# Kernel optimization log

Hardware: AMD Instinct MI355X
Metric: run time of the kernel (lower is better)

## Reference

```python
import jax, jax.numpy as jnp
import numpy as np

DIM = 1024
H = 16
HKV = 4
HD = DIM // H  # 64
GROUP = H // HKV
ROPE_BASE = 10000.0
B, T = 2, 2048


def rms_norm(x, eps):
    return x * jax.lax.rsqrt(jnp.mean(x * x, axis=-1, keepdims=True) + eps)


def apply_rotary(x, cos, sin):
    # x: [B, h, T, HD]; cos/sin: [1, 1, T, HD//2]
    half = x.shape[-1] // 2
    x1, x2 = x[..., :half], x[..., half:]
    return jnp.concatenate([x1 * cos + x2 * sin, -x1 * sin + x2 * cos], axis=-1)


def setup_inputs() -> dict:
    key = jax.random.key(0)
    ks = jax.random.split(key, 5)
    s = 0.02
    return {
        "x": jax.random.normal(ks[0], (B, T, DIM), dtype=jnp.float32),
        "Wq": jax.random.normal(ks[1], (DIM, DIM), dtype=jnp.float32) * s,
        "Wk": jax.random.normal(ks[2], (HKV * HD, DIM), dtype=jnp.float32) * s,
        "Wv": jax.random.normal(ks[3], (HKV * HD, DIM), dtype=jnp.float32) * s,
        "Wproj": jax.random.normal(ks[4], (DIM, DIM), dtype=jnp.float32) * s,
        "q_gain": jnp.full((H,), 12.0, dtype=jnp.float32),
    }


def reference(x, Wq, Wk, Wv, Wproj, q_gain):
    bsz, seqlen, dim = x.shape
    eps = jnp.asarray(jnp.finfo(x.dtype).eps, x.dtype)

    # double RMSNorm path: normalized input for q/k, raw input for v
    x_qk = rms_norm(x, eps)
    q = (x_qk @ Wq.T).reshape(bsz, seqlen, H, HD).transpose(0, 2, 1, 3)    # [B,H,T,D]
    k = (x_qk @ Wk.T).reshape(bsz, seqlen, HKV, HD).transpose(0, 2, 1, 3)  # [B,Hkv,T,D]
    v = (x @ Wv.T).reshape(bsz, seqlen, HKV, HD).transpose(0, 2, 1, 3)     # [B,Hkv,T,D]

    q = rms_norm(q, eps)
    k = rms_norm(k, eps)

    # rotary embeddings
    t = jnp.arange(seqlen, dtype=jnp.float32)
    inv_freq = 1.0 / (ROPE_BASE ** (jnp.arange(0, HD, 2, dtype=jnp.float32) / HD))
    freqs = jnp.outer(t, inv_freq)                       # [T, HD//2]
    cos = jnp.cos(freqs)[None, None].astype(x.dtype)
    sin = jnp.sin(freqs)[None, None].astype(x.dtype)
    q = apply_rotary(q, cos, sin)
    k = apply_rotary(k, cos, sin)

    # per-head gain on q
    q = q * q_gain.astype(q.dtype)[None, :, None, None]

    # GQA: expand kv heads to query heads
    k_r = jnp.repeat(k, GROUP, axis=1)  # [B,H,T,D]
    v_r = jnp.repeat(v, GROUP, axis=1)

    scale = 1.0 / np.sqrt(HD)
    scores = jnp.einsum("bhqd,bhkd->bhqk", q, k_r) * scale
    causal = jnp.tril(jnp.ones((seqlen, seqlen), dtype=bool))
    scores = jnp.where(causal[None, None], scores, jnp.asarray(-jnp.inf, scores.dtype))
    attn = jax.nn.softmax(scores, axis=-1)
    y = jnp.einsum("bhqk,bhkd->bhqd", attn, v_r)          # [B,H,T,D]

    # XSA: remove value-direction component from output
    y_bt = y.transpose(0, 2, 1, 3)                        # [B,T,H,D]
    v_bt = v.transpose(0, 2, 1, 3)                        # [B,T,Hkv,D]
    y_g = y_bt.reshape(bsz, seqlen, HKV, GROUP, HD)
    vnorm = jnp.sqrt(jnp.sum(v_bt * v_bt, axis=-1, keepdims=True))
    vn = (v_bt / jnp.maximum(vnorm, 1e-12))[..., None, :]  # [B,T,Hkv,1,D]
    proj = jnp.sum(y_g * vn, axis=-1, keepdims=True) * vn
    y_bt = (y_g - proj).reshape(bsz, seqlen, H, HD)

    return y_bt.reshape(bsz, seqlen, dim) @ Wproj.T
```

## Files before the change

kernel.cpp:

```cpp
#include <hip/hip_runtime.h>
#include <hip/hip_bf16.h>

typedef __attribute__((ext_vector_type(8))) short bf8v;
typedef __attribute__((ext_vector_type(4))) float f4v;
typedef __attribute__((ext_vector_type(4))) unsigned u4v;

#define MFMA16(a,b,c) __builtin_amdgcn_mfma_f32_16x16x32_bf16((a),(b),(c),0,0,0)

#define GLD16(gp, lp) __builtin_amdgcn_global_load_lds( \
    (const __attribute__((address_space(1))) void*)(gp), \
    (__attribute__((address_space(3))) void*)(lp), 16, 0, 0)

#define DIMC   1024
#define TSEQ   2048
#define NH     16
#define NKV    4
#define HDIM   64
#define RMS_EPS 1.1920929e-07f
#define QSCALE 0.1803368801111601f

__device__ __forceinline__ ushort f2bf(float f) {
  unsigned u = __builtin_bit_cast(unsigned, f);
  u = (u + 0x7FFFu + ((u >> 16) & 1u)) >> 16;
  return (ushort)u;
}
__device__ __forceinline__ float bf2f(ushort u) {
  return __builtin_bit_cast(float, (unsigned)u << 16);
}
__device__ __forceinline__ unsigned cvtpk(float lo, float hi) {
  unsigned r;
  asm("v_cvt_pk_bf16_f32 %0, %1, %2" : "=v"(r) : "v"(lo), "v"(hi));
  return r;
}

__global__ __launch_bounds__(256) void prep_all(
    const float* __restrict__ x,
    const float* __restrict__ Wq, const float* __restrict__ Wk,
    const float* __restrict__ Wv, const float* __restrict__ Wp,
    ushort* __restrict__ xhi, ushort* __restrict__ xlo,
    ushort* __restrict__ xb,
    ushort* __restrict__ wqkh, ushort* __restrict__ wqkl,
    ushort* __restrict__ wvb, ushort* __restrict__ wpb,
    float* __restrict__ cosT, float* __restrict__ sinT) {
  __shared__ float red[4];
  int bid = blockIdx.x, tid = threadIdx.x;
  if (bid < 4096) {
    int row = bid;
    int lane = tid & 63, w = tid >> 6;
    float4 v = ((const float4*)(x + (size_t)row * DIMC))[tid];
    float ss = v.x * v.x + v.y * v.y + v.z * v.z + v.w * v.w;
    for (int off = 32; off; off >>= 1) ss += __shfl_xor(ss, off);
    if (lane == 0) red[w] = ss;
    __syncthreads();
    float tot = red[0] + red[1] + red[2] + red[3];
    float rs = rsqrtf(tot * (1.0f / DIMC) + RMS_EPS);
    float n0 = v.x * rs, n1 = v.y * rs, n2 = v.z * rs, n3 = v.w * rs;
    ushort4 h, l, ob;
    h.x = f2bf(n0); l.x = f2bf(n0 - bf2f(h.x));
    h.y = f2bf(n1); l.y = f2bf(n1 - bf2f(h.y));
    h.z = f2bf(n2); l.z = f2bf(n2 - bf2f(h.z));
    h.w = f2bf(n3); l.w = f2bf(n3 - bf2f(h.w));
    ob.x = f2bf(v.x); ob.y = f2bf(v.y); ob.z = f2bf(v.z); ob.w = f2bf(v.w);
    ((ushort4*)(xhi + (size_t)row * DIMC))[tid] = h;
    ((ushort4*)(xlo + (size_t)row * DIMC))[tid] = l;
    ((ushort4*)(xb  + (size_t)row * DIMC))[tid] = ob;
    return;
  }
  int wb = bid - 4096;
  if (wb < 1280) {
    const float* src;
    size_t si, di;
    if (wb < 1024) { src = Wq; si = (size_t)wb * 256 + tid; di = si; }
    else { src = Wk; si = (size_t)(wb - 1024) * 256 + tid; di = 262144 + si; }
    float4 v = ((const float4*)src)[si];
    ushort4 h, l;
    h.x = f2bf(v.x); l.x = f2bf(v.x - bf2f(h.x));
    h.y = f2bf(v.y); l.y = f2bf(v.y - bf2f(h.y));
    h.z = f2bf(v.z); l.z = f2bf(v.z - bf2f(h.z));
    h.w = f2bf(v.w); l.w = f2bf(v.w - bf2f(h.w));
    ((ushort4*)wqkh)[di] = h;
    ((ushort4*)wqkl)[di] = l;
  } else if (wb < 2560) {
    const float* src;
    ushort* dst;
    int i;
    if (wb < 1536) { src = Wv; dst = wvb; i = (wb - 1280) * 256 + tid; }
    else           { src = Wp; dst = wpb; i = (wb - 1536) * 256 + tid; }
    float4 v = ((const float4*)src)[i];
    ushort4 o;
    o.x = f2bf(v.x); o.y = f2bf(v.y); o.z = f2bf(v.z); o.w = f2bf(v.w);
    ((ushort4*)dst)[i] = o;
  } else {
    int i = (wb - 2560) * 256 + tid;
    int t = i >> 5, j = i & 31;
    float inv = 1.0f / powf(10000.0f, (float)j * (1.0f / 32.0f));
    float f = (float)t * inv;
    cosT[i] = cosf(f);
    sinT[i] = sinf(f);
  }
}

__global__ __launch_bounds__(256, 3)
void gemm_qkv(const ushort* __restrict__ xhi, const ushort* __restrict__ xlo,
              const ushort* __restrict__ wqkh, const ushort* __restrict__ wqkl,
              float* __restrict__ QKf, ushort* __restrict__ QKc,
              const ushort* __restrict__ xb, const ushort* __restrict__ wvb,
              float* __restrict__ Vf) {
  __shared__ __align__(16) ushort lA[128 * 64];
  __shared__ __align__(16) ushort lB[128 * 64];
  const int bid = blockIdx.x;
  int u;
  bool big;
  if (bid < 256)      { big = true;  u = bid; }
  else if (bid < 448) { big = false; u = bid - 256; }
  else if (bid < 512) { big = true;  u = 256 + (bid - 448); }
  else                { big = false; u = 192 + (bid - 512); }

  const ushort *Ap0, *Bp0, *Ap1, *Bp1;
  float* Cf = QKf;
  int N = 1280, nsteps, mt, n0;
  if (big) {
    mt = u / 10; n0 = (u % 10) * 128;
    Ap0 = xlo; Bp0 = wqkh; Ap1 = xhi; Bp1 = wqkl; nsteps = 32;
  } else if (u < 320) {
    mt = u / 10; n0 = (u % 10) * 128;
    Ap0 = xhi; Bp0 = wqkh; Ap1 = Ap0; Bp1 = Bp0; nsteps = 16;
  } else {
    int v = u - 320; mt = v >> 1; n0 = (v & 1) * 128;
    Ap0 = xb; Bp0 = wvb; Ap1 = Ap0; Bp1 = Bp0; nsteps = 16;
    Cf = Vf; N = 256;
  }
  const int m0 = mt * 128;

  const int t = threadIdx.x;
  const int lane = t & 63, w = t >> 6;
  const int wr = w >> 1, wc = w & 1;
  const int l15 = lane & 15, lg = lane >> 4;
  const int srow = t >> 3, scp = t & 7;

  f4v acc[4][4] = {};

  for (int s = 0; s < nsteps; ++s) {
    const ushort* Ab = (s < 16) ? Ap0 : Ap1;
    const ushort* Bb = (s < 16) ? Bp0 : Bp1;
    const int kk = (s & 15) * 64;
    for (int i = 0; i < 4; ++i) {
      int row = srow + i * 32;
      int sc = scp ^ (row & 7);
      const ushort* ga = Ab + (size_t)(m0 + row) * DIMC + kk + sc * 8;
      const ushort* gb = Bb + (size_t)(n0 + row) * DIMC + kk + sc * 8;
      GLD16(ga, &lA[w * 512 + i * 2048]);
      GLD16(gb, &lB[w * 512 + i * 2048]);
    }
    __syncthreads();
    for (int kx = 0; kx < 2; ++kx) {
      bf8v af[4], bfr[4];
      for (int m = 0; m < 4; ++m) {
        int row = wr * 64 + m * 16 + l15;
        int ch = (kx * 4 + lg) ^ (row & 7);
        af[m] = *(const bf8v*)&lA[row * 64 + ch * 8];
      }
      for (int n = 0; n < 4; ++n) {
        int row = wc * 64 + n * 16 + l15;
        int ch = (kx * 4 + lg) ^ (row & 7);
        bfr[n] = *(const bf8v*)&lB[row * 64 + ch * 8];
      }
      for (int m = 0; m < 4; ++m)
        for (int n = 0; n < 4; ++n)
          acc[m][n] = MFMA16(af[m], bfr[n], acc[m][n]);
    }
    __syncthreads();
  }

  if (big) {
    for (int m = 0; m < 4; ++m)
      for (int n = 0; n < 4; ++n)
        for (int j = 0; j < 4; ++j) {
          int r = m0 + wr * 64 + m * 16 + lg * 4 + j;
          int c = n0 + wc * 64 + n * 16 + l15;
          QKc[(size_t)r * 1280 + c] = f2bf(acc[m][n][j]);
        }
  } else {
    for (int m = 0; m < 4; ++m)
      for (int n = 0; n < 4; ++n)
        for (int j = 0; j < 4; ++j) {
          int r = m0 + wr * 64 + m * 16 + lg * 4 + j;
          int c = n0 + wc * 64 + n * 16 + l15;
          Cf[(size_t)r * N + c] = acc[m][n][j];
        }
  }
}

__global__ __launch_bounds__(256, 2)
void gemm_bt(const ushort* __restrict__ A0, const ushort* __restrict__ B0,
             float* __restrict__ C, int N) {
  __shared__ __align__(16) ushort lA[128 * 64];
  __shared__ __align__(16) ushort lB[64 * 64];
  const int t = threadIdx.x;
  const int lane = t & 63, w = t >> 6;
  const int l15 = lane & 15, lg = lane >> 4;
  const int m0 = blockIdx.y * 128, n0 = blockIdx.x * 64;
  const int srow = t >> 3, scp = t & 7;

  f4v acc[2][4] = {};

  for (int k0 = 0; k0 < 1024; k0 += 64) {
    for (int i = 0; i < 4; ++i) {
      int row = srow + i * 32;
      int sc = scp ^ (row & 7);
      const ushort* ga = A0 + (size_t)(m0 + row) * DIMC + k0 + sc * 8;
      GLD16(ga, &lA[w * 512 + i * 2048]);
    }
    for (int i = 0; i < 2; ++i) {
      int row = srow + i * 32;
      int sc = scp ^ (row & 7);
      const ushort* gb = B0 + (size_t)(n0 + row) * DIMC + k0 + sc * 8;
      GLD16(gb, &lB[w * 512 + i * 2048]);
    }
    __syncthreads();
    for (int kx = 0; kx < 2; ++kx) {
      bf8v af[2], bfr[4];
      for (int m = 0; m < 2; ++m) {
        int row = w * 32 + m * 16 + l15;
        int ch = (kx * 4 + lg) ^ (row & 7);
        af[m] = *(const bf8v*)&lA[row * 64 + ch * 8];
      }
      for (int n = 0; n < 4; ++n) {
        int row = n * 16 + l15;
        int ch = (kx * 4 + lg) ^ (row & 7);
        bfr[n] = *(const bf8v*)&lB[row * 64 + ch * 8];
      }
      for (int m = 0; m < 2; ++m)
        for (int n = 0; n < 4; ++n)
          acc[m][n] = MFMA16(af[m], bfr[n], acc[m][n]);
    }
    __syncthreads();
  }

  for (int m = 0; m < 2; ++m)
    for (int n = 0; n < 4; ++n)
      for (int j = 0; j < 4; ++j) {
        int r = m0 + w * 32 + m * 16 + lg * 4 + j;
        int c = n0 + n * 16 + l15;
        C[(size_t)r * N + c] = acc[m][n][j];
      }
}

__global__ __launch_bounds__(256) void post_all(
    const float* __restrict__ QKf, const ushort* __restrict__ QKc,
    const float* __restrict__ cosT,
    const float* __restrict__ sinT, const float* __restrict__ qgain,
    ushort* __restrict__ qhi, ushort* __restrict__ qlo,
    ushort* __restrict__ kb16,
    const float* __restrict__ Vf, ushort* __restrict__ vt2,
    ushort* __restrict__ vhat_q) {
  __shared__ float lds[64][69];
  __shared__ float rnv[64];
  int bid = blockIdx.x;
  if (bid < 4096) {
    int m = bid;
    int b = m >> 11, tpos = m & 2047;
    int lane = threadIdx.x & 63, w = threadIdx.x >> 6;
    int d = lane, j = d & 31;
    float sgn = (d < 32) ? 1.0f : -1.0f;
    float c = cosT[tpos * 32 + j], s = sinT[tpos * 32 + j];

    for (int i = 0; i < 4; ++i) {
      int h = w * 4 + i;
      size_t base = (size_t)m * 1280 + h * HDIM + d;
      float q = QKf[base] + bf2f(QKc[base]);
      float ss = q * q;
      for (int off = 32; off; off >>= 1) ss += __shfl_xor(ss, off);
      float rs = rsqrtf(ss * (1.0f / HDIM) + RMS_EPS);
      float qn = q * rs;
      float partner = __shfl_xor(qn, 32);
      float ro = (qn * c + sgn * partner * s) * (qgain[h] * QSCALE);
      ushort hi = f2bf(ro);
      ushort lo = f2bf(ro - bf2f(hi));
      size_t idx = (((size_t)b * NH + h) * TSEQ + tpos) * HDIM + d;
      qhi[idx] = hi;
      qlo[idx] = lo;
    }
    {
      int kv = w;
      size_t base = (size_t)m * 1280 + 1024 + kv * HDIM + d;
      float k = QKf[base] + bf2f(QKc[base]);
      float ss = k * k;
      for (int off = 32; off; off >>= 1) ss += __shfl_xor(ss, off);
      float rs = rsqrtf(ss * (1.0f / HDIM) + RMS_EPS);
      float kn = k * rs;
      float partner = __shfl_xor(kn, 32);
      float ro = kn * c + sgn * partner * s;
      kb16[((size_t)(b * NKV + kv) * TSEQ + tpos) * HDIM + d] = f2bf(ro);
    }
    return;
  }
  {
    int vb = bid - 4096;
    int bkv = vb >> 5, tt = vb & 31;
    int b = bkv >> 2, kv = bkv & 3;
    int tid = threadIdx.x;
    for (int i = 0; i < 16; ++i) {
      int idx = i * 256 + tid;
      int tloc = idx >> 6, d = idx & 63;
      lds[d][tloc] = Vf[((size_t)(b * TSEQ + tt * 64 + tloc)) * 256 + kv * 64 + d];
    }
    __syncthreads();
    {
      int t = tid >> 2, prt = tid & 3;
      float ssum = 0.f;
      for (int dd = 0; dd < 16; ++dd) {
        float v = lds[prt * 16 + dd][t];
        ssum += v * v;
      }
      ssum += __shfl_xor(ssum, 1);
      ssum += __shfl_xor(ssum, 2);
      if (prt == 0) rnv[t] = 1.0f / fmaxf(sqrtf(ssum), 1e-12f);
    }
    __syncthreads();
    for (int i = 0; i < 16; ++i) {
      int idx = i * 256 + tid;
      int d = idx >> 6, tloc = idx & 63;
      vt2[(size_t)bkv * (TSEQ * 64) + tt * 4096 + d * 64 + tloc] = f2bf(lds[d][tloc]);
    }
    for (int i = 0; i < 16; ++i) {
      int idx = i * 256 + tid;
      int tloc = idx >> 6, d = idx & 63;
      vhat_q[((size_t)bkv * TSEQ + tt * 64 + tloc) * 64 + d] =
          f2bf(lds[d][tloc] * rnv[tloc]);
    }
  }
}

#define E(s,t,k,l) ((unsigned)(s) | ((unsigned)(t) << 8) | \
                    ((unsigned)(k) << 16) | ((unsigned)(l) << 24))
__global__ __launch_bounds__(256, 5) void attn_chunk(
    const ushort* __restrict__ qhi, const ushort* __restrict__ qlo,
    const ushort* __restrict__ kb16, const ushort* __restrict__ vt2,
    ushort* __restrict__ pyb, float* __restrict__ pml) {
  static const unsigned LUT[80] = {
    E(76,31,0,8), E(77,31,8,8), E(78,31,16,8), E(79,31,24,8),
    E(72,30,0,8), E(73,30,8,8), E(74,30,16,8),
    E(68,29,0,8), E(69,29,8,8), E(64,28,0,8),
    E(45,23,0,8), E(46,23,8,8), E(47,23,16,8),
    E(42,22,0,8), E(43,22,8,8), E(39,21,0,8),
    E(22,15,0,8), E(23,15,8,8), E(20,14,0,8), E(7,7,0,8),
    E(75,30,24,7), E(70,29,16,7), E(71,29,23,7),
    E(65,28,8,7), E(66,28,15,7), E(67,28,22,7),
    E(60,27,0,7), E(61,27,7,7), E(62,27,14,7), E(63,27,21,7),
    E(56,26,0,7), E(57,26,7,7), E(58,26,14,7),
    E(52,25,0,7), E(53,25,7,7), E(48,24,0,7),
    E(44,22,16,7), E(40,21,8,7), E(41,21,15,7),
    E(36,20,0,7), E(37,20,7,7), E(38,20,14,7),
    E(33,19,0,7), E(34,19,7,7), E(30,18,0,7),
    E(21,14,8,7), E(18,13,0,7), E(19,13,7,7), E(16,12,0,7), E(6,6,0,7),
    E(59,26,21,6), E(54,25,14,6), E(55,25,20,6),
    E(49,24,7,6), E(50,24,13,6), E(51,24,19,6),
    E(35,19,14,6), E(31,18,7,6), E(32,18,13,6),
    E(27,17,0,6), E(28,17,6,6), E(29,17,12,6),
    E(24,16,0,6), E(25,16,6,6),
    E(17,12,7,6), E(14,11,0,6), E(15,11,6,6), E(12,10,0,6), E(5,5,0,6),
    E(26,16,12,5), E(13,10,6,5), E(10,9,0,5), E(11,9,5,5),
    E(8,8,0,5), E(4,4,0,5),
    E(9,8,5,4), E(3,3,0,4),
    E(2,2,0,3), E(1,1,0,2), E(0,0,0,1)
  };
  __shared__ __align__(16) ushort lk[2][64 * 64];
  __shared__ __align__(16) ushort lv[2][64 * 64];
  const int t = threadIdx.x;
  const int lane = t & 63, w = t >> 6;
  const int bid = blockIdx.x;
  const int combo = bid & 31;
  const unsigned e = LUT[bid >> 5];
  const int slot = e & 255;
  const int tile = (e >> 8) & 31;
  const int kb0 = (e >> 16) & 31;
  const int len = (int)(e >> 24);

  const int xcd = combo & 7, g = (combo >> 3) & 3;
  const int b = xcd >> 2, kv = xcd & 3, h = kv * 4 + g;
  const int l15 = lane & 15, lg = lane >> 4;
  const int q0 = tile * 64 + w * 16;
  const int t3 = t >> 3, tc8 = t & 7;
  const int rx = l15 & 7;
  const bool odd = (lg & 1);

  const size_t qoff = (((size_t)(b * NH + h)) * TSEQ + q0 + l15) * HDIM;
  bf8v bq0h = *(const bf8v*)(qhi + qoff + lg * 8);
  bf8v bq1h = *(const bf8v*)(qhi + qoff + 32 + lg * 8);
  bf8v bq0l = *(const bf8v*)(qlo + qoff + lg * 8);
  bf8v bq1l = *(const bf8v*)(qlo + qoff + 32 + lg * 8);

  const ushort* kb = kb16 + (size_t)(b * NKV + kv) * TSEQ * 64;
  const ushort* vb = vt2 + (size_t)(b * NKV + kv) * TSEQ * 64;

#define STAGE(BUF, KT) do { \
    _Pragma("unroll") \
    for (int i = 0; i < 2; ++i) { \
      int row = i * 32 + t3; \
      int sc = tc8 ^ (row & 7); \
      GLD16(kb + (size_t)((KT) * 64 + row) * 64 + sc * 8, \
            &lk[BUF][(i * 32 + (w << 3)) * 64]); \
      GLD16(vb + (size_t)(KT) * 4096 + row * 64 + sc * 8, \
            &lv[BUF][(i * 32 + (w << 3)) * 64]); \
    } } while (0)

  STAGE(0, kb0);

  f4v y[4] = {};
  float mrow = -1e30f, lrow = 0.f;

#pragma unroll 1
  for (int itc = 0; itc < len; ++itc) {
    const int cur = itc & 1;
    const int kt = kb0 + itc;
    __syncthreads();
    if (itc + 1 < len) STAGE(cur ^ 1, kt + 1);

    const ushort* lkc = &lk[cur][0];
    const ushort* lvc = &lv[cur][0];
    const int kv0 = kt * 64;

    f4v s4[4];
    __builtin_amdgcn_s_setprio(1);
#pragma unroll
    for (int n = 0; n < 4; ++n) {
      const ushort* krow = lkc + (n * 16 + l15) * 64;
      bf8v kh0 = *(const bf8v*)&krow[((0 + lg) ^ rx) * 8];
      bf8v kh1 = *(const bf8v*)&krow[((4 + lg) ^ rx) * 8];
      f4v z = {};
      f4v acc = MFMA16(kh0, bq0h, z);
      acc = MFMA16(kh1, bq1h, acc);
      acc = MFMA16(kh0, bq0l, acc);
      acc = MFMA16(kh1, bq1l, acc);
      s4[n] = acc;
    }
    __builtin_amdgcn_s_setprio(0);

    const bool need_mask = (kt == tile);
    float mloc = -1e30f;
#pragma unroll
    for (int n = 0; n < 4; ++n)
#pragma unroll
      for (int j = 0; j < 4; ++j) {
        float v = s4[n][j];
        if (need_mask && (kv0 + n * 16 + lg * 4 + j > q0 + l15)) v = -1e30f;
        s4[n][j] = v;
        mloc = fmaxf(mloc, v);
      }
    if (__any(mloc > mrow + 11.5f)) {
      float mf = fmaxf(mloc, __shfl_xor(mloc, 16));
      mf = fmaxf(mf, __shfl_xor(mf, 32));
      float mnew = fmaxf(mrow, mf);
      float scf = exp2f(mrow - mnew);
      lrow *= scf;
#pragma unroll
      for (int n = 0; n < 4; ++n) y[n] *= scf;
      mrow = mnew;
    }
#pragma unroll
    for (int n = 0; n < 4; ++n)
#pragma unroll
      for (int j = 0; j < 4; ++j) {
        float e2 = exp2f(s4[n][j] - mrow);
        s4[n][j] = e2;
        lrow += e2;
      }

    unsigned d0a = cvtpk(s4[0][0], s4[0][1]), d0b = cvtpk(s4[0][2], s4[0][3]);
    unsigned d1a = cvtpk(s4[1][0], s4[1][1]), d1b = cvtpk(s4[1][2], s4[1][3]);
    unsigned d2a = cvtpk(s4[2][0], s4[2][1]), d2b = cvtpk(s4[2][2], s4[2][3]);
    unsigned d3a = cvtpk(s4[3][0], s4[3][1]), d3b = cvtpk(s4[3][2], s4[3][3]);
    asm("v_permlane32_swap_b32 %0, %1" : "+v"(d0a), "+v"(d1a));
    asm("v_permlane32_swap_b32 %0, %1" : "+v"(d0b), "+v"(d1b));
    asm("v_permlane32_swap_b32 %0, %1" : "+v"(d2a), "+v"(d3a));
    asm("v_permlane32_swap_b32 %0, %1" : "+v"(d2b), "+v"(d3b));
    unsigned sa0 = (unsigned)__shfl_xor((int)d0a, 16);
    unsigned sb0 = (unsigned)__shfl_xor((int)d1a, 16);
    unsigned sa1 = (unsigned)__shfl_xor((int)d0b, 16);
    unsigned sb1 = (unsigned)__shfl_xor((int)d1b, 16);
    unsigned sa2 = (unsigned)__shfl_xor((int)d2a, 16);
    unsigned sb2 = (unsigned)__shfl_xor((int)d3a, 16);
    unsigned sa3 = (unsigned)__shfl_xor((int)d2b, 16);
    unsigned sb3 = (unsigned)__shfl_xor((int)d3b, 16);
    u4v u0 = { odd ? sb0 : d0a, odd ? sb1 : d0b,
               odd ? d1a : sa0, odd ? d1b : sa1 };
    u4v u1 = { odd ? sb2 : d2a, odd ? sb3 : d2b,
               odd ? d3a : sa2, odd ? d3b : sa3 };
    bf8v pb0 = __builtin_bit_cast(bf8v, u0);
    bf8v pb1 = __builtin_bit_cast(bf8v, u1);

    __builtin_amdgcn_s_setprio(1);
#pragma unroll
    for (int n = 0; n < 4; ++n) {
      const ushort* vrow = lvc + (n * 16 + l15) * 64;
      bf8v va0 = *(const bf8v*)&vrow[((0 + lg) ^ rx) * 8];
      bf8v va1 = *(const bf8v*)&vrow[((4 + lg) ^ rx) * 8];
      y[n] = MFMA16(va0, pb0, y[n]);
      y[n] = MFMA16(va1, pb1, y[n]);
    }
    __builtin_amdgcn_s_setprio(0);
  }
#undef STAGE

  {
    lrow += __shfl_xor(lrow, 16);
    lrow += __shfl_xor(lrow, 32);
    const int pslot = combo * 80 + slot;
    ushort* pb = pyb + (size_t)pslot * 4096;
    const int q = w * 16 + l15;
#pragma unroll
    for (int n = 0; n < 4; ++n) {
      uint2 pk;
      pk.x = cvtpk(y[n][0], y[n][1]);
      pk.y = cvtpk(y[n][2], y[n][3]);
      *(uint2*)&pb[q * 64 + n * 16 + lg * 4] = pk;
    }
    if (lane < 16) {
      float* mlp = pml + (size_t)pslot * 128;
      mlp[q] = mrow;
      mlp[64 + q] = lrow;
    }
  }
}
#undef E

__global__ __launch_bounds__(256) void combine_kern(
    const ushort* __restrict__ pyb, const float* __restrict__ pml,
    const ushort* __restrict__ vhat_q, ushort* __restrict__ ytil) {
  const int bid = blockIdx.x;
  const int combo = bid & 31, tile = bid >> 5;
  const int xcd = combo & 7, g = (combo >> 3) & 3;
  const int b = xcd >> 2, kv = xcd & 3, h = kv * 4 + g;
  const int nch = (tile + 8) >> 3;
  const int sb = (tile < 8) ? tile
               : (tile < 16) ? 8 + ((tile - 8) << 1)
               : (tile < 24) ? 24 + 3 * (tile - 16)
                             : 48 + ((tile - 24) << 2);
  const int tid = threadIdx.x;
  const int q = tid >> 2, ds = (tid & 3) * 16;
  const int q0 = tile * 64;

  float m[4], l[4];
#pragma unroll
  for (int ci = 0; ci < 4; ++ci) {
    if (ci < nch) {
      const float* mlp = pml + (size_t)(combo * 80 + sb + ci) * 128;
      m[ci] = mlp[q];
      l[ci] = mlp[64 + q];
    } else { m[ci] = -1e30f; l[ci] = 0.f; }
  }
  float M = fmaxf(fmaxf(m[0], m[1]), fmaxf(m[2], m[3]));
  float y[16] = {};
  float ltot = 0.f;
#pragma unroll
  for (int ci = 0; ci < 4; ++ci) {
    if (ci < nch) {
      float sc = exp2f(m[ci] - M);
      ltot += l[ci] * sc;
      const ushort* pb = pyb + (size_t)(combo * 80 + sb + ci) * 4096 + q * 64 + ds;
      bf8v p0 = *(const bf8v*)pb;
      bf8v p1 = *(const bf8v*)(pb + 8);
#pragma unroll
      for (int dd = 0; dd < 8; ++dd) {
        y[dd] += sc * bf2f((ushort)p0[dd]);
        y[8 + dd] += sc * bf2f((ushort)p1[dd]);
      }
    }
  }
  float inv = 1.0f / ltot;
  const ushort* vh = vhat_q + ((size_t)(b * NKV + kv) * TSEQ + q0 + q) * 64 + ds;
  bf8v v0 = *(const bf8v*)vh;
  bf8v v1 = *(const bf8v*)(vh + 8);
  float vv[16];
  float dp = 0.f;
#pragma unroll
  for (int dd = 0; dd < 8; ++dd) {
    vv[dd] = bf2f((ushort)v0[dd]);
    vv[8 + dd] = bf2f((ushort)v1[dd]);
  }
#pragma unroll
  for (int dd = 0; dd < 16; ++dd) {
    y[dd] *= inv;
    dp += y[dd] * vv[dd];
  }
  dp += __shfl_xor(dp, 1);
  dp += __shfl_xor(dp, 2);
  bf8v o0, o1;
#pragma unroll
  for (int dd = 0; dd < 8; ++dd) {
    o0[dd] = (short)f2bf(y[dd] - dp * vv[dd]);
    o1[dd] = (short)f2bf(y[8 + dd] - dp * vv[8 + dd]);
  }
  ushort* yo = ytil + ((size_t)(b * TSEQ + q0 + q)) * DIMC + h * HDIM + ds;
  *(bf8v*)yo = o0;
  *(bf8v*)(yo + 8) = o1;
}

extern "C" void kernel_launch(void* const* d_in, const int* in_sizes, int n_in,
                              void* d_out, int out_size, void* d_ws, size_t ws_size,
                              hipStream_t stream) {
  (void)in_sizes; (void)n_in; (void)out_size; (void)ws_size;
  const float* x  = (const float*)d_in[0];
  const float* Wq = (const float*)d_in[1];
  const float* Wk = (const float*)d_in[2];
  const float* Wv = (const float*)d_in[3];
  const float* Wp = (const float*)d_in[4];
  const float* qg = (const float*)d_in[5];
  float* out = (float*)d_out;
  char* ws = (char*)d_ws;
  const size_t KB = 1024, MB = 1ull << 20;

  ushort* xhi = (ushort*)(ws);
  ushort* xlo = (ushort*)(ws + 8 * MB);
  ushort* xb  = (ushort*)(ws + 16 * MB);
  ushort* wqkh = (ushort*)(ws + 24 * MB);
  ushort* wqkl = (ushort*)(ws + 26 * MB + 512 * KB);
  ushort* wvb = (ushort*)(ws + 29 * MB);
  ushort* wpb = (ushort*)(ws + 29 * MB + 512 * KB);
  float*  cosT = (float*)(ws + 31 * MB + 512 * KB);
  float*  sinT = (float*)(ws + 31 * MB + 768 * KB);
  float*  QKf  = (float*)(ws + 32 * MB);
  ushort* kb16 = (ushort*)(ws + 52 * MB);
  ushort* vt2  = (ushort*)(ws + 54 * MB);

  float*  Vf   = out;
  ushort* QKc  = (ushort*)((char*)out + 4 * MB);
  ushort* vhat_q = (ushort*)((char*)out + 14 * MB);
  ushort* qhb  = xhi;
  ushort* qlb  = xlo;
  ushort* ytil = xb;
  ushort* pyb = (ushort*)(ws + 32 * MB);
  float*  pml = (float*)(ws + 56 * MB);

  prep_all<<<6912, 256, 0, stream>>>(x, Wq, Wk, Wv, Wp, xhi, xlo, xb,
                                     wqkh, wqkl, wvb, wpb, cosT, sinT);

  gemm_qkv<<<704, 256, 0, stream>>>(xhi, xlo, wqkh, wqkl, QKf, QKc,
                                    xb, wvb, Vf);

  post_all<<<4352, 256, 0, stream>>>(QKf, QKc, cosT, sinT, qg, qhb, qlb, kb16,
                                     Vf, vt2, vhat_q);
  attn_chunk<<<2560, 256, 0, stream>>>(qhb, qlb, kb16, vt2, pyb, pml);
  combine_kern<<<1024, 256, 0, stream>>>(pyb, pml, vhat_q, ytil);
  gemm_bt<<<dim3(16, 32), 256, 0, stream>>>(ytil, wpb, out, 1024);
}
```

Baseline: 141.9 us.

## Process two 64-row query tiles per attention block to reuse staged K/V

Result: slower. 220.3 us (+55.2%).

```diff
diff --git a/kernel.cpp b/kernel.cpp
--- a/kernel.cpp
+++ b/kernel.cpp
@@ -332,38 +332,89 @@
   }
 }
 
+__device__ __forceinline__ void softmax_redist(
+    f4v s4[4], f4v y[4], float& mrow, float& lrow,
+    int kv0, int qcol, bool need_mask, bool odd, int lg,
+    bf8v& pb0, bf8v& pb1) {
+  float mloc = -1e30f;
+#pragma unroll
+  for (int n = 0; n < 4; ++n)
+#pragma unroll
+    for (int j = 0; j < 4; ++j) {
+      float v = s4[n][j];
+      if (need_mask && (kv0 + n * 16 + lg * 4 + j > qcol)) v = -1e30f;
+      s4[n][j] = v;
+      mloc = fmaxf(mloc, v);
+    }
+  if (__any(mloc > mrow + 11.5f)) {
+    float mf = fmaxf(mloc, __shfl_xor(mloc, 16));
+    mf = fmaxf(mf, __shfl_xor(mf, 32));
+    float mnew = fmaxf(mrow, mf);
+    float scf = exp2f(mrow - mnew);
+    lrow *= scf;
+#pragma unroll
+    for (int n = 0; n < 4; ++n) y[n] *= scf;
+    mrow = mnew;
+  }
+#pragma unroll
+  for (int n = 0; n < 4; ++n)
+#pragma unroll
+    for (int j = 0; j < 4; ++j) {
+      float e2 = exp2f(s4[n][j] - mrow);
+      s4[n][j] = e2;
+      lrow += e2;
+    }
+  unsigned d0a = cvtpk(s4[0][0], s4[0][1]), d0b = cvtpk(s4[0][2], s4[0][3]);
+  unsigned d1a = cvtpk(s4[1][0], s4[1][1]), d1b = cvtpk(s4[1][2], s4[1][3]);
+  unsigned d2a = cvtpk(s4[2][0], s4[2][1]), d2b = cvtpk(s4[2][2], s4[2][3]);
+  unsigned d3a = cvtpk(s4[3][0], s4[3][1]), d3b = cvtpk(s4[3][2], s4[3][3]);
+  asm("v_permlane32_swap_b32 %0, %1" : "+v"(d0a), "+v"(d1a));
+  asm("v_permlane32_swap_b32 %0, %1" : "+v"(d0b), "+v"(d1b));
+  asm("v_permlane32_swap_b32 %0, %1" : "+v"(d2a), "+v"(d3a));
+  asm("v_permlane32_swap_b32 %0, %1" : "+v"(d2b), "+v"(d3b));
+  unsigned sa0 = (unsigned)__shfl_xor((int)d0a, 16);
+  unsigned sb0 = (unsigned)__shfl_xor((int)d1a, 16);
+  unsigned sa1 = (unsigned)__shfl_xor((int)d0b, 16);
+  unsigned sb1 = (unsigned)__shfl_xor((int)d1b, 16);
+  unsigned sa2 = (unsigned)__shfl_xor((int)d2a, 16);
+  unsigned sb2 = (unsigned)__shfl_xor((int)d3a, 16);
+  unsigned sa3 = (unsigned)__shfl_xor((int)d2b, 16);
+  unsigned sb3 = (unsigned)__shfl_xor((int)d3b, 16);
+  u4v u0 = { odd ? sb0 : d0a, odd ? sb1 : d0b,
+             odd ? d1a : sa0, odd ? d1b : sa1 };
+  u4v u1 = { odd ? sb2 : d2a, odd ? sb3 : d2b,
+             odd ? d3a : sa2, odd ? d3b : sa3 };
+  pb0 = __builtin_bit_cast(bf8v, u0);
+  pb1 = __builtin_bit_cast(bf8v, u1);
+}
+
 #define E(s,t,k,l) ((unsigned)(s) | ((unsigned)(t) << 8) | \
                     ((unsigned)(k) << 16) | ((unsigned)(l) << 24))
-__global__ __launch_bounds__(256, 5) void attn_chunk(
+__global__ __launch_bounds__(256, 4) void attn_chunk(
     const ushort* __restrict__ qhi, const ushort* __restrict__ qlo,
     const ushort* __restrict__ kb16, const ushort* __restrict__ vt2,
     ushort* __restrict__ pyb, float* __restrict__ pml) {
-  static const unsigned LUT[80] = {
-    E(76,31,0,8), E(77,31,8,8), E(78,31,16,8), E(79,31,24,8),
-    E(72,30,0,8), E(73,30,8,8), E(74,30,16,8),
-    E(68,29,0,8), E(69,29,8,8), E(64,28,0,8),
-    E(45,23,0,8), E(46,23,8,8), E(47,23,16,8),
-    E(42,22,0,8), E(43,22,8,8), E(39,21,0,8),
-    E(22,15,0,8), E(23,15,8,8), E(20,14,0,8), E(7,7,0,8),
-    E(75,30,24,7), E(70,29,16,7), E(71,29,23,7),
-    E(65,28,8,7), E(66,28,15,7), E(67,28,22,7),
-    E(60,27,0,7), E(61,27,7,7), E(62,27,14,7), E(63,27,21,7),
-    E(56,26,0,7), E(57,26,7,7), E(58,26,14,7),
-    E(52,25,0,7), E(53,25,7,7), E(48,24,0,7),
-    E(44,22,16,7), E(40,21,8,7), E(41,21,15,7),
-    E(36,20,0,7), E(37,20,7,7), E(38,20,14,7),
-    E(33,19,0,7), E(34,19,7,7), E(30,18,0,7),
-    E(21,14,8,7), E(18,13,0,7), E(19,13,7,7), E(16,12,0,7), E(6,6,0,7),
-    E(59,26,21,6), E(54,25,14,6), E(55,25,20,6),
-    E(49,24,7,6), E(50,24,13,6), E(51,24,19,6),
-    E(35,19,14,6), E(31,18,7,6), E(32,18,13,6),
-    E(27,17,0,6), E(28,17,6,6), E(29,17,12,6),
-    E(24,16,0,6), E(25,16,6,6),
-    E(17,12,7,6), E(14,11,0,6), E(15,11,6,6), E(12,10,0,6), E(5,5,0,6),
-    E(26,16,12,5), E(13,10,6,5), E(10,9,0,5), E(11,9,5,5),
-    E(8,8,0,5), E(4,4,0,5),
-    E(9,8,5,4), E(3,3,0,4),
-    E(2,2,0,3), E(1,1,0,2), E(0,0,0,1)
+  static const unsigned LUT[40] = {
+    E(36,15,0,8), E(37,15,8,8), E(38,15,16,8), E(39,15,24,8),
+    E(32,14,0,8), E(33,14,8,8),
+    E(21,11,0,8), E(22,11,8,8), E(23,11,16,8),
+    E(18,10,0,8),
+    E(10,7,0,8), E(11,7,8,8),
+    E(3,3,0,8),
+    E(34,14,16,7), E(35,14,23,7),
+    E(28,13,0,7), E(29,13,7,7), E(30,13,14,7), E(31,13,21,7),
+    E(24,12,0,7), E(25,12,7,7),
+    E(19,10,8,7), E(20,10,15,7),
+    E(15,9,0,7), E(16,9,7,7),
+    E(8,6,0,7), E(9,6,7,7),
+    E(26,12,14,6), E(27,12,20,6),
+    E(17,9,14,6),
+    E(12,8,0,6), E(13,8,6,6), E(14,8,12,6),
+    E(6,5,0,6), E(7,5,6,6),
+    E(2,2,0,6),
+    E(4,4,0,5), E(5,4,5,5),
+    E(1,1,0,4),
+    E(0,0,0,2)
   };
   __shared__ __align__(16) ushort lk[2][64 * 64];
   __shared__ __align__(16) ushort lv[2][64 * 64];
@@ -380,16 +431,24 @@
   const int xcd = combo & 7, g = (combo >> 3) & 3;
   const int b = xcd >> 2, kv = xcd & 3, h = kv * 4 + g;
   const int l15 = lane & 15, lg = lane >> 4;
-  const int q0 = tile * 64 + w * 16;
+  const int qa = tile * 128 + w * 16;
+  const int qb = qa + 64;
+  const int ktA_last = 2 * tile;
+  const int ktB_last = 2 * tile + 1;
   const int t3 = t >> 3, tc8 = t & 7;
   const int rx = l15 & 7;
   const bool odd = (lg & 1);
 
-  const size_t qoff = (((size_t)(b * NH + h)) * TSEQ + q0 + l15) * HDIM;
-  bf8v bq0h = *(const bf8v*)(qhi + qoff + lg * 8);
-  bf8v bq1h = *(const bf8v*)(qhi + qoff + 32 + lg * 8);
-  bf8v bq0l = *(const bf8v*)(qlo + qoff + lg * 8);
-  bf8v bq1l = *(const bf8v*)(qlo + qoff + 32 + lg * 8);
+  const size_t qoffA = (((size_t)(b * NH + h)) * TSEQ + qa + l15) * HDIM;
+  const size_t qoffB = qoffA + 64 * HDIM;
+  bf8v bqA0h = *(const bf8v*)(qhi + qoffA + lg * 8);
+  bf8v bqA1h = *(const bf8v*)(qhi + qoffA + 32 + lg * 8);
+  bf8v bqA0l = *(const bf8v*)(qlo + qoffA + lg * 8);
+  bf8v bqA1l = *(const bf8v*)(qlo + qoffA + 32 + lg * 8);
+  bf8v bqB0h = *(const bf8v*)(qhi + qoffB + lg * 8);
+  bf8v bqB1h = *(const bf8v*)(qhi + qoffB + 32 + lg * 8);
+  bf8v bqB0l = *(const bf8v*)(qlo + qoffB + lg * 8);
+  bf8v bqB1l = *(const bf8v*)(qlo + qoffB + 32 + lg * 8);
 
   const ushort* kb = kb16 + (size_t)(b * NKV + kv) * TSEQ * 64;
   const ushort* vb = vt2 + (size_t)(b * NKV + kv) * TSEQ * 64;
@@ -407,8 +466,9 @@
 
   STAGE(0, kb0);
 
-  f4v y[4] = {};
-  float mrow = -1e30f, lrow = 0.f;
+  f4v yA[4] = {}, yB[4] = {};
+  float mrowA = -1e30f, lrowA = 0.f;
+  float mrowB = -1e30f, lrowB = 0.f;
 
 #pragma unroll 1
   for (int itc = 0; itc < len; ++itc) {
@@ -420,75 +480,41 @@
     const ushort* lkc = &lk[cur][0];
     const ushort* lvc = &lv[cur][0];
     const int kv0 = kt * 64;
-
-    f4v s4[4];
+    const bool doA = (kt <= ktA_last);
+
+    f4v sA[4], sB[4];
     __builtin_amdgcn_s_setprio(1);
 #pragma unroll
     for (int n = 0; n < 4; ++n) {
       const ushort* krow = lkc + (n * 16 + l15) * 64;
       bf8v kh0 = *(const bf8v*)&krow[((0 + lg) ^ rx) * 8];
       bf8v kh1 = *(const bf8v*)&krow[((4 + lg) ^ rx) * 8];
-      f4v z = {};
-      f4v acc = MFMA16(kh0, bq0h, z);
-      acc = MFMA16(kh1, bq1h, acc);
-      acc = MFMA16(kh0, bq0l, acc);
-      acc = MFMA16(kh1, bq1l, acc);
-      s4[n] = acc;
+      if (doA) {
+        f4v z = {};
+        f4v acc = MFMA16(kh0, bqA0h, z);
+        acc = MFMA16(kh1, bqA1h, acc);
+        acc = MFMA16(kh0, bqA0l, acc);
+        acc = MFMA16(kh1, bqA1l, acc);
+        sA[n] = acc;
+      }
+      {
+        f4v z = {};
+        f4v acc = MFMA16(kh0, bqB0h, z);
+        acc = MFMA16(kh1, bqB1h, acc);
+        acc = MFMA16(kh0, bqB0l, acc);
+        acc = MFMA16(kh1, bqB1l, acc);
+        sB[n] = acc;
+      }
     }
     __builtin_amdgcn_s_setprio(0);
 
-    const bool need_mask = (kt == tile);
-    float mloc = -1e30f;
-#pragma unroll
-    for (int n = 0; n < 4; ++n)
-#pragma unroll
-      for (int j = 0; j < 4; ++j) {
-        float v = s4[n][j];
-        if (need_mask && (kv0 + n * 16 + lg * 4 + j > q0 + l15)) v = -1e30f;
-        s4[n][j] = v;
-        mloc = fmaxf(mloc, v);
-      }
-    if (__any(mloc > mrow + 11.5f)) {
-      float mf = fmaxf(mloc, __shfl_xor(mloc, 16));
-      mf = fmaxf(mf, __shfl_xor(mf, 32));
-      float mnew = fmaxf(mrow, mf);
-      float scf = exp2f(mrow - mnew);
-      lrow *= scf;
-#pragma unroll
-      for (int n = 0; n < 4; ++n) y[n] *= scf;
-      mrow = mnew;
-    }
-#pragma unroll
-    for (int n = 0; n < 4; ++n)
-#pragma unroll
-      for (int j = 0; j < 4; ++j) {
-        float e2 = exp2f(s4[n][j] - mrow);
-        s4[n][j] = e2;
-        lrow += e2;
-      }
-
-    unsigned d0a = cvtpk(s4[0][0], s4[0][1]), d0b = cvtpk(s4[0][2], s4[0][3]);
-    unsigned d1a = cvtpk(s4[1][0], s4[1][1]), d1b = cvtpk(s4[1][2], s4[1][3]);
-    unsigned d2a = cvtpk(s4[2][0], s4[2][1]), d2b = cvtpk(s4[2][2], s4[2][3]);
-    unsigned d3a = cvtpk(s4[3][0], s4[3][1]), d3b = cvtpk(s4[3][2], s4[3][3]);
-    asm("v_permlane32_swap_b32 %0, %1" : "+v"(d0a), "+v"(d1a));
-    asm("v_permlane32_swap_b32 %0, %1" : "+v"(d0b), "+v"(d1b));
-    asm("v_permlane32_swap_b32 %0, %1" : "+v"(d2a), "+v"(d3a));
-    asm("v_permlane32_swap_b32 %0, %1" : "+v"(d2b), "+v"(d3b));
-    unsigned sa0 = (unsigned)__shfl_xor((int)d0a, 16);
-    unsigned sb0 = (unsigned)__shfl_xor((int)d1a, 16);
-    unsigned sa1 = (unsigned)__shfl_xor((int)d0b, 16);
-    unsigned sb1 = (unsigned)__shfl_xor((int)d1b, 16);
-    unsigned sa2 = (unsigned)__shfl_xor((int)d2a, 16);
-    unsigned sb2 = (unsigned)__shfl_xor((int)d3a, 16);
-    unsigned sa3 = (unsigned)__shfl_xor((int)d2b, 16);
-    unsigned sb3 = (unsigned)__shfl_xor((int)d3b, 16);
-    u4v u0 = { odd ? sb0 : d0a, odd ? sb1 : d0b,
-               odd ? d1a : sa0, odd ? d1b : sa1 };
-    u4v u1 = { odd ? sb2 : d2a, odd ? sb3 : d2b,
-               odd ? d3a : sa2, odd ? d3b : sa3 };
-    bf8v pb0 = __builtin_bit_cast(bf8v, u0);
-    bf8v pb1 = __builtin_bit_cast(bf8v, u1);
+    bf8v pbA0 = {}, pbA1 = {};
+    if (doA)
+      softmax_redist(sA, yA, mrowA, lrowA, kv0, qa + l15,
+                     kt == ktA_last, odd, lg, pbA0, pbA1);
+    bf8v pbB0, pbB1;
+    softmax_redist(sB, yB, mrowB, lrowB, kv0, qb + l15,
+                   kt == ktB_last, odd, lg, pbB0, pbB1);
 
     __builtin_amdgcn_s_setprio(1);
 #pragma unroll
@@ -496,30 +522,42 @@
       const ushort* vrow = lvc + (n * 16 + l15) * 64;
       bf8v va0 = *(const bf8v*)&vrow[((0 + lg) ^ rx) * 8];
       bf8v va1 = *(const bf8v*)&vrow[((4 + lg) ^ rx) * 8];
-      y[n] = MFMA16(va0, pb0, y[n]);
-      y[n] = MFMA16(va1, pb1, y[n]);
+      if (doA) {
+        yA[n] = MFMA16(va0, pbA0, yA[n]);
+        yA[n] = MFMA16(va1, pbA1, yA[n]);
+      }
+      yB[n] = MFMA16(va0, pbB0, yB[n]);
+      yB[n] = MFMA16(va1, pbB1, yB[n]);
     }
     __builtin_amdgcn_s_setprio(0);
   }
 #undef STAGE
 
   {
-    lrow += __shfl_xor(lrow, 16);
-    lrow += __shfl_xor(lrow, 32);
-    const int pslot = combo * 80 + slot;
-    ushort* pb = pyb + (size_t)pslot * 4096;
-    const int q = w * 16 + l15;
+    lrowA += __shfl_xor(lrowA, 16);
+    lrowA += __shfl_xor(lrowA, 32);
+    lrowB += __shfl_xor(lrowB, 16);
+    lrowB += __shfl_xor(lrowB, 32);
+    const int pslot = combo * 40 + slot;
+    ushort* pb = pyb + (size_t)pslot * 8192;
+    const int qA = w * 16 + l15;
+    const int qB = 64 + qA;
 #pragma unroll
     for (int n = 0; n < 4; ++n) {
-      uint2 pk;
-      pk.x = cvtpk(y[n][0], y[n][1]);
-      pk.y = cvtpk(y[n][2], y[n][3]);
-      *(uint2*)&pb[q * 64 + n * 16 + lg * 4] = pk;
+      uint2 pkA, pkB;
+      pkA.x = cvtpk(yA[n][0], yA[n][1]);
+      pkA.y = cvtpk(yA[n][2], yA[n][3]);
+      pkB.x = cvtpk(yB[n][0], yB[n][1]);
+      pkB.y = cvtpk(yB[n][2], yB[n][3]);
+      *(uint2*)&pb[qA * 64 + n * 16 + lg * 4] = pkA;
+      *(uint2*)&pb[qB * 64 + n * 16 + lg * 4] = pkB;
     }
     if (lane < 16) {
-      float* mlp = pml + (size_t)pslot * 128;
-      mlp[q] = mrow;
-      mlp[64 + q] = lrow;
+      float* mlp = pml + (size_t)pslot * 256;
+      mlp[qA] = mrowA;
+      mlp[128 + qA] = lrowA;
+      mlp[qB] = mrowB;
+      mlp[128 + qB] = lrowB;
     }
   }
 }
@@ -529,25 +567,27 @@
     const ushort* __restrict__ pyb, const float* __restrict__ pml,
     const ushort* __restrict__ vhat_q, ushort* __restrict__ ytil) {
   const int bid = blockIdx.x;
-  const int combo = bid & 31, tile = bid >> 5;
+  const int combo = bid & 31, ht = bid >> 5;
+  const int tile = ht >> 1;
   const int xcd = combo & 7, g = (combo >> 3) & 3;
   const int b = xcd >> 2, kv = xcd & 3, h = kv * 4 + g;
-  const int nch = (tile + 8) >> 3;
-  const int sb = (tile < 8) ? tile
-               : (tile < 16) ? 8 + ((tile - 8) << 1)
-               : (tile < 24) ? 24 + 3 * (tile - 16)
-                             : 48 + ((tile - 24) << 2);
+  const int nch = (tile >> 2) + 1;
+  const int sb = (tile < 4) ? tile
+               : (tile < 8) ? 4 + 2 * (tile - 4)
+               : (tile < 12) ? 12 + 3 * (tile - 8)
+                             : 24 + 4 * (tile - 12);
   const int tid = threadIdx.x;
   const int q = tid >> 2, ds = (tid & 3) * 16;
-  const int q0 = tile * 64;
+  const int qp = (ht & 1) * 64 + q;
+  const int q0 = ht * 64;
 
   float m[4], l[4];
 #pragma unroll
   for (int ci = 0; ci < 4; ++ci) {
     if (ci < nch) {
-      const float* mlp = pml + (size_t)(combo * 80 + sb + ci) * 128;
-      m[ci] = mlp[q];
-      l[ci] = mlp[64 + q];
+      const float* mlp = pml + (size_t)(combo * 40 + sb + ci) * 256;
+      m[ci] = mlp[qp];
+      l[ci] = mlp[128 + qp];
     } else { m[ci] = -1e30f; l[ci] = 0.f; }
   }
   float M = fmaxf(fmaxf(m[0], m[1]), fmaxf(m[2], m[3]));
@@ -558,7 +598,7 @@
     if (ci < nch) {
       float sc = exp2f(m[ci] - M);
       ltot += l[ci] * sc;
-      const ushort* pb = pyb + (size_t)(combo * 80 + sb + ci) * 4096 + q * 64 + ds;
+      const ushort* pb = pyb + (size_t)(combo * 40 + sb + ci) * 8192 + qp * 64 + ds;
       bf8v p0 = *(const bf8v*)pb;
       bf8v p1 = *(const bf8v*)(pb + 8);
 #pragma unroll
@@ -641,7 +681,7 @@
 
   post_all<<<4352, 256, 0, stream>>>(QKf, QKc, cosT, sinT, qg, qhb, qlb, kb16,
                                      Vf, vt2, vhat_q);
-  attn_chunk<<<2560, 256, 0, stream>>>(qhb, qlb, kb16, vt2, pyb, pml);
+  attn_chunk<<<1280, 256, 0, stream>>>(qhb, qlb, kb16, vt2, pyb, pml);
   combine_kern<<<1024, 256, 0, stream>>>(pyb, pml, vhat_q, ytil);
   gemm_bt<<<dim3(16, 32), 256, 0, stream>>>(ytil, wpb, out, 1024);
 }
```
